# Kernel tuning notes

Hardware: AMD Instinct MI355X
Metric: run time of the kernel (lower is better)

The kernel has to match this reference:

```python
import jax, jax.numpy as jnp
import numpy as np
import math

S, B, H, NH = 2048, 1, 4096, 32
D = H // NH  # 128 head dim


def rotate_half(x):
    x1, x2 = x[..., : x.shape[-1] // 2], x[..., x.shape[-1] // 2 :]
    return jnp.concatenate((-x2, x1), axis=-1)


def setup_inputs() -> dict:
    key = jax.random.key(0)
    k1, k2, k3, k4, k5 = jax.random.split(key, 5)
    hidden_states = jax.random.normal(k1, (S, B, H), dtype=jnp.float32)
    position_ids = jnp.broadcast_to(jnp.arange(S, dtype=jnp.int32)[None, :], (B, S))
    # causal mask: True = masked (upper triangle above diagonal)
    attention_mask = jnp.triu(jnp.ones((S, S), dtype=bool), k=1)[None, None]
    W_qkv = jax.random.normal(k2, (H, 3 * H), dtype=jnp.float32) * 0.02
    b_qkv = jax.random.normal(k3, (3 * H,), dtype=jnp.float32) * 0.02
    W_dense = jax.random.normal(k4, (H, H), dtype=jnp.float32) * 0.02
    b_dense = jax.random.normal(k5, (H,), dtype=jnp.float32) * 0.02
    return {
        "hidden_states": hidden_states,
        "position_ids": position_ids,
        "attention_mask": attention_mask,
        "W_qkv": W_qkv,
        "b_qkv": b_qkv,
        "W_dense": W_dense,
        "b_dense": b_dense,
        "layer_id": 27,
    }


def reference(hidden_states, position_ids, attention_mask, W_qkv, b_qkv, W_dense, b_dense, layer_id):
    s, b, h = hidden_states.shape
    nh, d = NH, D
    # QKV projection: [s, b, 3h] -> [s, b, nh, 3d] -> split
    mixed = hidden_states @ W_qkv + b_qkv
    mixed = mixed.reshape(s, b, nh, 3 * d)
    q, k, v = jnp.split(mixed, 3, axis=-1)  # each [s, b, nh, d]
    # rotary embedding indexed by position_ids (transposed to [s, b])
    pos = position_ids.T  # [s, b]
    inv_freq = 1.0 / (10000.0 ** (jnp.arange(0, d, 2, dtype=jnp.float32) / d))
    freqs = pos[..., None].astype(jnp.float32) * inv_freq  # [s, b, d/2]
    emb = jnp.concatenate((freqs, freqs), axis=-1)  # [s, b, d]
    cos = jnp.cos(emb)[:, :, None, :]  # [s, b, 1, d]
    sin = jnp.sin(emb)[:, :, None, :]
    q = q * cos + rotate_half(q) * sin
    k = k * cos + rotate_half(k) * sin
    # attention with per-layer scaling coeff (cancels in softmax except mask fill)
    coeff = jnp.float32(layer_id + 1)
    q_scaled = q / (math.sqrt(d) * coeff)
    scores = jnp.einsum("sbnd,tbnd->bnst", q_scaled, k)  # [b, nh, s, s]
    scores = jnp.where(attention_mask, jnp.float32(-10000.0), scores) * coeff
    probs = jax.nn.softmax(scores, axis=-1)
    ctx = jnp.einsum("bnst,tbnd->sbnd", probs, v).reshape(s, b, h)
    out = ctx @ W_dense + b_dense
    return out
```

## Files before the change

kernel.cpp:

```cpp
#include <hip/hip_runtime.h>

#define S_LEN 2048
#define HID   4096
#define NHEAD 32
#define DHEAD 128
#define H3    12288

typedef __attribute__((ext_vector_type(8))) __bf16 bf16x8;
typedef __attribute__((ext_vector_type(4))) __bf16 bf16x4;
typedef __attribute__((ext_vector_type(4))) float  f32x4;
typedef __attribute__((ext_vector_type(16))) float f32x16;

__device__ __forceinline__ void gl_lds16(const void* g, void* l) {
  __builtin_amdgcn_global_load_lds(
      (const __attribute__((address_space(1))) void*)g,
      (__attribute__((address_space(3))) void*)l, 16, 0, 0);
}

__global__ void cvt_f32_bf16(const float* __restrict__ in, __bf16* __restrict__ out, int n4) {
  int i = blockIdx.x * blockDim.x + threadIdx.x;
  if (i >= n4) return;
  float4 v = ((const float4*)in)[i];
  bf16x4 o;
  o.x = (__bf16)v.x; o.y = (__bf16)v.y; o.z = (__bf16)v.z; o.w = (__bf16)v.w;
  ((bf16x4*)out)[i] = o;
}

__global__ void transpose_cvt(const float* __restrict__ in, __bf16* __restrict__ out, int R, int C) {
  __shared__ float t[64][65];
  const int tid = threadIdx.x;
  const int r0 = blockIdx.y * 64, c0 = blockIdx.x * 64;
#pragma unroll
  for (int p = 0; p < 4; ++p) {
    int r = p * 16 + (tid >> 4);
    int c4 = (tid & 15) * 4;
    float4 v = *(const float4*)(in + (size_t)(r0 + r) * C + c0 + c4);
    t[r][c4] = v.x; t[r][c4 + 1] = v.y; t[r][c4 + 2] = v.z; t[r][c4 + 3] = v.w;
  }
  __syncthreads();
#pragma unroll
  for (int p = 0; p < 4; ++p) {
    int c = p * 16 + (tid >> 4);
    int rg = (tid & 15) * 4;
    bf16x4 o;
    o.x = (__bf16)t[rg][c]; o.y = (__bf16)t[rg + 1][c];
    o.z = (__bf16)t[rg + 2][c]; o.w = (__bf16)t[rg + 3][c];
    *(bf16x4*)(out + (size_t)(c0 + c) * R + r0 + rg) = o;
  }
}

__global__ void rope_kernel(__bf16* __restrict__ q, __bf16* __restrict__ k,
                            const int* __restrict__ pos) {
  int idx = blockIdx.x * 256 + threadIdx.x;
  int j = idx & 63;
  int hs = idx >> 6;
  int s = hs & (S_LEN - 1);
  float p = (float)pos[s];
  float invf = __expf(-(float)j * (9.210340371976184f / 64.f));
  float a = p * invf;
  float c, sn;
  __sincosf(a, &sn, &c);
  size_t base = (size_t)hs * 128;
  float x1 = (float)q[base + j], x2 = (float)q[base + j + 64];
  q[base + j]      = (__bf16)(x1 * c - x2 * sn);
  q[base + j + 64] = (__bf16)(x2 * c + x1 * sn);
  x1 = (float)k[base + j]; x2 = (float)k[base + j + 64];
  k[base + j]      = (__bf16)(x1 * c - x2 * sn);
  k[base + j + 64] = (__bf16)(x2 * c + x1 * sn);
}

template <int EPI>
__global__ __launch_bounds__(256, 2)
void gemm32(const __bf16* __restrict__ A, const __bf16* __restrict__ BT,
            const float* __restrict__ bias, int K,
            __bf16* __restrict__ outq, __bf16* __restrict__ outk,
            __bf16* __restrict__ outvt, float* __restrict__ outf) {
  const int tid = threadIdx.x;
  const int lane = tid & 63;
  const int wave = tid >> 6;
  const int bm = blockIdx.x * 256;
  const int bn = blockIdx.y * 128;

  __shared__ char lds[49152];
  char* Ab = lds;
  char* Bb = lds + 32768;

  f32x16 acc[4][2] = {};

  const int wm = (wave >> 1) * 128;
  const int wn = (wave & 1) * 64;
  const int l31 = lane & 31;
  const int hi = lane >> 5;

  const int sr = tid >> 3;
  const int scb = ((tid & 7) * 16) ^ ((sr & 7) << 4);
  const int K2 = K * 2;
  const char* Arow = (const char*)A + (size_t)(bm + sr) * K2 + scb;
  const char* Brow = (const char*)BT + (size_t)(bn + sr) * K2 + scb;

  for (int k0 = 0; k0 < K; k0 += 64) {
    const char* a_src = Arow + (size_t)k0 * 2;
    const char* b_src = Brow + (size_t)k0 * 2;
    char* a_dst = Ab + wave * 1024;
    char* b_dst = Bb + wave * 1024;
#pragma unroll
    for (int i = 0; i < 8; ++i)
      gl_lds16(a_src + (size_t)i * 32 * K2, a_dst + i * 4096);
#pragma unroll
    for (int i = 0; i < 4; ++i)
      gl_lds16(b_src + (size_t)i * 32 * K2, b_dst + i * 4096);
    __syncthreads();
#pragma unroll
    for (int kk = 0; kk < 4; ++kk) {
      const int cbase = kk * 32 + (hi << 4);
      bf16x8 af[4], bfr[2];
#pragma unroll
      for (int m = 0; m < 4; ++m) {
        const int row = wm + m * 32 + l31;
        af[m] = *(const bf16x8*)(Ab + row * 128 + (cbase ^ ((row & 7) << 4)));
      }
#pragma unroll
      for (int n = 0; n < 2; ++n) {
        const int row = wn + n * 32 + l31;
        bfr[n] = *(const bf16x8*)(Bb + row * 128 + (cbase ^ ((row & 7) << 4)));
      }
#pragma unroll
      for (int m = 0; m < 4; ++m)
#pragma unroll
        for (int n = 0; n < 2; ++n)
          acc[m][n] = __builtin_amdgcn_mfma_f32_32x32x16_bf16(af[m], bfr[n], acc[m][n], 0, 0, 0);
    }
    __syncthreads();
  }

  if (EPI == 0) {
    const int route = (bn >> 7) % 3;
    const int head = bn / 384;
#pragma unroll
    for (int n = 0; n < 2; ++n) {
      const int d = wn + n * 32 + l31;
      const float bv = bias[bn + d];
#pragma unroll
      for (int m = 0; m < 4; ++m) {
        if (route == 2) {
#pragma unroll
          for (int qd = 0; qd < 4; ++qd) {
            const int srow = bm + wm + m * 32 + qd * 8 + (hi << 2);
            bf16x4 o;
            o.x = (__bf16)(acc[m][n][qd * 4 + 0] + bv);
            o.y = (__bf16)(acc[m][n][qd * 4 + 1] + bv);
            o.z = (__bf16)(acc[m][n][qd * 4 + 2] + bv);
            o.w = (__bf16)(acc[m][n][qd * 4 + 3] + bv);
            *(bf16x4*)(outvt + ((size_t)head * 128 + d) * S_LEN + srow) = o;
          }
        } else {
          __bf16* dst = (route == 0 ? outq : outk) + (size_t)head * S_LEN * 128;
#pragma unroll
          for (int r = 0; r < 16; ++r) {
            const int srow = bm + wm + m * 32 + (r & 3) + 8 * (r >> 2) + (hi << 2);
            dst[(size_t)srow * 128 + d] = (__bf16)(acc[m][n][r] + bv);
          }
        }
      }
    }
  } else {
#pragma unroll
    for (int n = 0; n < 2; ++n) {
      const int col = bn + wn + n * 32 + l31;
      const float bv = bias[col];
#pragma unroll
      for (int m = 0; m < 4; ++m)
#pragma unroll
        for (int r = 0; r < 16; ++r) {
          const int srow = bm + wm + m * 32 + (r & 3) + 8 * (r >> 2) + (hi << 2);
          outf[(size_t)srow * HID + col] = acc[m][n][r] + bv;
        }
    }
  }
}

__global__ __launch_bounds__(256, 2)
void attn_kernel(const __bf16* __restrict__ q, const __bf16* __restrict__ k,
                 const __bf16* __restrict__ vt, __bf16* __restrict__ ctx) {
  const int p = blockIdx.x, h = blockIdx.y;
  const int tid = threadIdx.x, lane = tid & 63, wave = tid >> 6;
  __shared__ __bf16 Ks[64 * 128];
  __shared__ __bf16 Vs[128 * 64];
  __shared__ __bf16 Ps[4][16 * 64];
  char* Kb = (char*)Ks;
  char* Vb = (char*)Vs;
  char* Pb = (char*)(Ps[wave]);

  const __bf16* qh = q + (size_t)h * S_LEN * 128;
  const __bf16* kh = k + (size_t)h * S_LEN * 128;
  const __bf16* vh = vt + (size_t)h * 128 * S_LEN;

  const int cl = lane & 15, rbase = (lane >> 4) << 2;

  const int krow = tid >> 4, kcol = (tid & 15) * 16;
  const int kcs = kcol ^ ((krow & 7) << 4);
  const int vrow = tid >> 3, vcol = (tid & 7) * 16;
  const int vcs = vcol ^ ((vrow & 7) << 4);

  for (int half = 0; half < 2; ++half) {
    const int qt = half ? (31 - p) : p;
    const int qrow0 = qt * 64 + wave * 16;

    bf16x8 qf[4];
#pragma unroll
    for (int kk = 0; kk < 4; ++kk)
      qf[kk] = *(const bf16x8*)(qh + (size_t)(qrow0 + cl) * 128 + kk * 32 + ((lane >> 4) << 3));

    f32x4 oacc[8] = {};
    float mrow[4], lrow[4];
#pragma unroll
    for (int r = 0; r < 4; ++r) { mrow[r] = -1e30f; lrow[r] = 0.f; }

    for (int j = 0; j <= qt; ++j) {
      {
        const char* src = (const char*)(kh + (size_t)(j * 64 + krow) * 128) + kcs;
        char* dst = Kb + wave * 1024;
#pragma unroll
        for (int i = 0; i < 4; ++i)
          gl_lds16(src + (size_t)i * 16 * 256, dst + i * 4096);
      }
      {
        const char* src = (const char*)(vh + (size_t)vrow * S_LEN + j * 64) + vcs;
        char* dst = Vb + wave * 1024;
#pragma unroll
        for (int i = 0; i < 4; ++i)
          gl_lds16(src + (size_t)i * 32 * (S_LEN * 2), dst + i * 4096);
      }
      __syncthreads();

      f32x4 sacc[4] = {};
#pragma unroll
      for (int kk = 0; kk < 4; ++kk) {
        bf16x8 bk[4];
#pragma unroll
        for (int n = 0; n < 4; ++n) {
          int row = n * 16 + cl;
          int cb = (kk * 64 + ((lane >> 4) << 4)) ^ ((row & 7) << 4);
          bk[n] = *(const bf16x8*)(Kb + row * 256 + cb);
        }
#pragma unroll
        for (int n = 0; n < 4; ++n)
          sacc[n] = __builtin_amdgcn_mfma_f32_16x16x32_bf16(qf[kk], bk[n], sacc[n], 0, 0, 0);
      }

      float pmax[4];
#pragma unroll
      for (int r = 0; r < 4; ++r) pmax[r] = -1e30f;
      if (j == qt) {
#pragma unroll
        for (int n = 0; n < 4; ++n) {
          const int col = n * 16 + cl;
#pragma unroll
          for (int r = 0; r < 4; ++r) {
            const int row = wave * 16 + rbase + r;
            float sv = sacc[n][r] * 0.08838834764831845f;
            sv = (col > row) ? -1e30f : sv;
            sacc[n][r] = sv;
            pmax[r] = fmaxf(pmax[r], sv);
          }
        }
      } else {
#pragma unroll
        for (int n = 0; n < 4; ++n)
#pragma unroll
          for (int r = 0; r < 4; ++r) {
            float sv = sacc[n][r] * 0.08838834764831845f;
            sacc[n][r] = sv;
            pmax[r] = fmaxf(pmax[r], sv);
          }
      }
#pragma unroll
      for (int xm = 1; xm < 16; xm <<= 1)
#pragma unroll
        for (int r = 0; r < 4; ++r)
          pmax[r] = fmaxf(pmax[r], __shfl_xor(pmax[r], xm, 64));
#pragma unroll
      for (int r = 0; r < 4; ++r) {
        const float mnew = fmaxf(mrow[r], pmax[r]);
        const float alpha = __expf(mrow[r] - mnew);
        mrow[r] = mnew;
        float psum = 0.f;
#pragma unroll
        for (int n = 0; n < 4; ++n) {
          float pe = __expf(sacc[n][r] - mnew);
          sacc[n][r] = pe;
          psum += pe;
        }
#pragma unroll
        for (int xm = 1; xm < 16; xm <<= 1)
          psum += __shfl_xor(psum, xm, 64);
        lrow[r] = lrow[r] * alpha + psum;
#pragma unroll
        for (int nd = 0; nd < 8; ++nd)
          oacc[nd][r] *= alpha;
      }

#pragma unroll
      for (int n = 0; n < 4; ++n) {
        const int colb = (n * 16 + cl) * 2;
#pragma unroll
        for (int r = 0; r < 4; ++r) {
          const int row = rbase + r;
          *(__bf16*)(Pb + row * 128 + (colb ^ ((row & 7) << 4))) = (__bf16)sacc[n][r];
        }
      }

#pragma unroll
      for (int kk = 0; kk < 2; ++kk) {
        bf16x8 pa, bv[8];
        {
          int row = cl;
          int cb = (kk * 64 + ((lane >> 4) << 4)) ^ ((row & 7) << 4);
          pa = *(const bf16x8*)(Pb + row * 128 + cb);
        }
#pragma unroll
        for (int nd = 0; nd < 8; ++nd) {
          int row = nd * 16 + cl;
          int cb = (kk * 64 + ((lane >> 4) << 4)) ^ ((row & 7) << 4);
          bv[nd] = *(const bf16x8*)(Vb + row * 128 + cb);
        }
#pragma unroll
        for (int nd = 0; nd < 8; ++nd)
          oacc[nd] = __builtin_amdgcn_mfma_f32_16x16x32_bf16(pa, bv[nd], oacc[nd], 0, 0, 0);
      }
      __syncthreads();
    }

#pragma unroll
    for (int nd = 0; nd < 8; ++nd) {
      const int d = nd * 16 + cl;
#pragma unroll
      for (int r = 0; r < 4; ++r) {
        const int srow = qrow0 + rbase + r;
        ctx[(size_t)srow * HID + h * 128 + d] = (__bf16)(oacc[nd][r] / lrow[r]);
      }
    }
  }
}

extern "C" void kernel_launch(void* const* d_in, const int* in_sizes, int n_in,
                              void* d_out, int out_size, void* d_ws, size_t ws_size,
                              hipStream_t stream) {
  const float* hs = (const float*)d_in[0];
  const int* pos = (const int*)d_in[1];
  const float* wqkv = (const float*)d_in[3];
  const float* bqkv = (const float*)d_in[4];
  const float* wd = (const float*)d_in[5];
  const float* bd = (const float*)d_in[6];
  float* out = (float*)d_out;

  char* ws = (char*)d_ws;
  const size_t MB = 1024ull * 1024ull;
  if (ws_size < 160 * MB) return;
  __bf16* wT  = (__bf16*)(ws);
  __bf16* xb  = (__bf16*)(ws + 96 * MB);
  __bf16* qb_ = (__bf16*)(ws + 112 * MB);
  __bf16* kb_ = (__bf16*)(ws + 128 * MB);
  __bf16* vtb = (__bf16*)(ws + 144 * MB);

  cvt_f32_bf16<<<8192, 256, 0, stream>>>(hs, xb, 2097152);
  transpose_cvt<<<dim3(192, 64), 256, 0, stream>>>(wqkv, wT, 4096, 12288);
  gemm32<0><<<dim3(8, 96), 256, 0, stream>>>(xb, wT, bqkv, 4096, qb_, kb_, vtb, nullptr);
  rope_kernel<<<16384, 256, 0, stream>>>(qb_, kb_, pos);
  transpose_cvt<<<dim3(64, 64), 256, 0, stream>>>(wd, wT, 4096, 4096);
  attn_kernel<<<dim3(16, 32), 256, 0, stream>>>(qb_, kb_, vtb, xb);
  gemm32<1><<<dim3(8, 32), 256, 0, stream>>>(xb, wT, bd, 4096, nullptr, nullptr, nullptr, out);
}
```

Before: 500.9 us.

## Fold softmax scale into RoPE, add lazy rescale, use 128x128 dense GEMM

The 1/sqrt(d) scale is folded into Q during the RoPE pass, which removes a multiply per score in attention. The online softmax now skips the running-max update and accumulator rescale when every row's new max stays within 8 of the old one. The output projection moves to a new 128x128-tile GEMM built on 16x16x32 MFMA, launched on a 16x32 grid instead of 8x32 so more blocks fill the CUs. Tradeoffs: scaling Q before rounding to bf16 shifts rounding slightly, skipped rescales rely on exp staying bounded, and the new GEMM has no double buffering.

```diff
diff --git a/kernel.cpp b/kernel.cpp
--- a/kernel.cpp
+++ b/kernel.cpp
@@ -60,13 +60,93 @@
   float a = p * invf;
   float c, sn;
   __sincosf(a, &sn, &c);
+  const float SC = 0.08838834764831845f;
   size_t base = (size_t)hs * 128;
   float x1 = (float)q[base + j], x2 = (float)q[base + j + 64];
-  q[base + j]      = (__bf16)(x1 * c - x2 * sn);
-  q[base + j + 64] = (__bf16)(x2 * c + x1 * sn);
+  q[base + j]      = (__bf16)((x1 * c - x2 * sn) * SC);
+  q[base + j + 64] = (__bf16)((x2 * c + x1 * sn) * SC);
   x1 = (float)k[base + j]; x2 = (float)k[base + j + 64];
   k[base + j]      = (__bf16)(x1 * c - x2 * sn);
   k[base + j + 64] = (__bf16)(x2 * c + x1 * sn);
+}
+
+template <int EPI>
+__global__ __launch_bounds__(256, 2)
+void gemm_bf16(const __bf16* __restrict__ A, const __bf16* __restrict__ BT,
+               const float* __restrict__ bias, int K,
+               float* __restrict__ outf) {
+  const int tid = threadIdx.x;
+  const int lane = tid & 63;
+  const int wave = tid >> 6;
+  const int bm = blockIdx.x * 128;
+  const int bn = blockIdx.y * 128;
+
+  __shared__ __bf16 As[128 * 64];
+  __shared__ __bf16 Bs[128 * 64];
+  char* Ab = (char*)As;
+  char* Bb = (char*)Bs;
+
+  f32x4 acc[4][4] = {};
+
+  const int wm = (wave >> 1) * 64;
+  const int wn = (wave & 1) * 64;
+
+  const int sr = tid >> 3;
+  const int sc = (tid & 7) * 16;
+  const int scs = sc ^ ((sr & 7) << 4);
+
+  const char* Arow = (const char*)(A + (size_t)(bm + sr) * K) + scs;
+  const char* Brow = (const char*)(BT + (size_t)(bn + sr) * K) + scs;
+
+  for (int k0 = 0; k0 < K; k0 += 64) {
+    const char* a_src = Arow + (size_t)k0 * 2;
+    const char* b_src = Brow + (size_t)k0 * 2;
+    char* a_dst = Ab + wave * 1024;
+    char* b_dst = Bb + wave * 1024;
+#pragma unroll
+    for (int i = 0; i < 4; ++i) {
+      gl_lds16(a_src + (size_t)i * 32 * K * 2, a_dst + i * 4096);
+      gl_lds16(b_src + (size_t)i * 32 * K * 2, b_dst + i * 4096);
+    }
+    __syncthreads();
+#pragma unroll
+    for (int kk = 0; kk < 2; ++kk) {
+      bf16x8 af[4], bfr[4];
+#pragma unroll
+      for (int m = 0; m < 4; ++m) {
+        int row = wm + m * 16 + (lane & 15);
+        int cb = (kk * 64 + ((lane >> 4) << 4)) ^ ((row & 7) << 4);
+        af[m] = *(const bf16x8*)(Ab + row * 128 + cb);
+      }
+#pragma unroll
+      for (int n = 0; n < 4; ++n) {
+        int row = wn + n * 16 + (lane & 15);
+        int cb = (kk * 64 + ((lane >> 4) << 4)) ^ ((row & 7) << 4);
+        bfr[n] = *(const bf16x8*)(Bb + row * 128 + cb);
+      }
+#pragma unroll
+      for (int m = 0; m < 4; ++m)
+#pragma unroll
+        for (int n = 0; n < 4; ++n)
+          acc[m][n] = __builtin_amdgcn_mfma_f32_16x16x32_bf16(af[m], bfr[n], acc[m][n], 0, 0, 0);
+    }
+    __syncthreads();
+  }
+
+  const int rbase = (lane >> 4) << 2;
+  const int cl = lane & 15;
+#pragma unroll
+  for (int n = 0; n < 4; ++n) {
+    const int col = bn + wn + n * 16 + cl;
+    const float bv = bias[col];
+#pragma unroll
+    for (int m = 0; m < 4; ++m) {
+      const int srow = bm + wm + m * 16 + rbase;
+#pragma unroll
+      for (int r = 0; r < 4; ++r)
+        outf[(size_t)(srow + r) * HID + col] = acc[m][n][r] + bv;
+    }
+  }
 }
 
 template <int EPI>
@@ -74,7 +154,7 @@
 void gemm32(const __bf16* __restrict__ A, const __bf16* __restrict__ BT,
             const float* __restrict__ bias, int K,
             __bf16* __restrict__ outq, __bf16* __restrict__ outk,
-            __bf16* __restrict__ outvt, float* __restrict__ outf) {
+            __bf16* __restrict__ outvt) {
   const int tid = threadIdx.x;
   const int lane = tid & 63;
   const int wave = tid >> 6;
@@ -133,48 +213,33 @@
     __syncthreads();
   }
 
-  if (EPI == 0) {
-    const int route = (bn >> 7) % 3;
-    const int head = bn / 384;
-#pragma unroll
-    for (int n = 0; n < 2; ++n) {
-      const int d = wn + n * 32 + l31;
-      const float bv = bias[bn + d];
-#pragma unroll
-      for (int m = 0; m < 4; ++m) {
-        if (route == 2) {
-#pragma unroll
-          for (int qd = 0; qd < 4; ++qd) {
-            const int srow = bm + wm + m * 32 + qd * 8 + (hi << 2);
-            bf16x4 o;
-            o.x = (__bf16)(acc[m][n][qd * 4 + 0] + bv);
-            o.y = (__bf16)(acc[m][n][qd * 4 + 1] + bv);
-            o.z = (__bf16)(acc[m][n][qd * 4 + 2] + bv);
-            o.w = (__bf16)(acc[m][n][qd * 4 + 3] + bv);
-            *(bf16x4*)(outvt + ((size_t)head * 128 + d) * S_LEN + srow) = o;
-          }
-        } else {
-          __bf16* dst = (route == 0 ? outq : outk) + (size_t)head * S_LEN * 128;
-#pragma unroll
-          for (int r = 0; r < 16; ++r) {
-            const int srow = bm + wm + m * 32 + (r & 3) + 8 * (r >> 2) + (hi << 2);
-            dst[(size_t)srow * 128 + d] = (__bf16)(acc[m][n][r] + bv);
-          }
-        }
-      }
-    }
-  } else {
-#pragma unroll
-    for (int n = 0; n < 2; ++n) {
-      const int col = bn + wn + n * 32 + l31;
-      const float bv = bias[col];
-#pragma unroll
-      for (int m = 0; m < 4; ++m)
+  const int route = (bn >> 7) % 3;
+  const int head = bn / 384;
+#pragma unroll
+  for (int n = 0; n < 2; ++n) {
+    const int d = wn + n * 32 + l31;
+    const float bv = bias[bn + d];
+#pragma unroll
+    for (int m = 0; m < 4; ++m) {
+      if (route == 2) {
+#pragma unroll
+        for (int qd = 0; qd < 4; ++qd) {
+          const int srow = bm + wm + m * 32 + qd * 8 + (hi << 2);
+          bf16x4 o;
+          o.x = (__bf16)(acc[m][n][qd * 4 + 0] + bv);
+          o.y = (__bf16)(acc[m][n][qd * 4 + 1] + bv);
+          o.z = (__bf16)(acc[m][n][qd * 4 + 2] + bv);
+          o.w = (__bf16)(acc[m][n][qd * 4 + 3] + bv);
+          *(bf16x4*)(outvt + ((size_t)head * 128 + d) * S_LEN + srow) = o;
+        }
+      } else {
+        __bf16* dst = (route == 0 ? outq : outk) + (size_t)head * S_LEN * 128;
 #pragma unroll
         for (int r = 0; r < 16; ++r) {
           const int srow = bm + wm + m * 32 + (r & 3) + 8 * (r >> 2) + (hi << 2);
-          outf[(size_t)srow * HID + col] = acc[m][n][r] + bv;
-        }
+          dst[(size_t)srow * 128 + d] = (__bf16)(acc[m][n][r] + bv);
+        }
+      }
     }
   }
 }
@@ -258,8 +323,7 @@
 #pragma unroll
           for (int r = 0; r < 4; ++r) {
             const int row = wave * 16 + rbase + r;
-            float sv = sacc[n][r] * 0.08838834764831845f;
-            sv = (col > row) ? -1e30f : sv;
+            float sv = (col > row) ? -1e30f : sacc[n][r];
             sacc[n][r] = sv;
             pmax[r] = fmaxf(pmax[r], sv);
           }
@@ -268,36 +332,53 @@
 #pragma unroll
         for (int n = 0; n < 4; ++n)
 #pragma unroll
-          for (int r = 0; r < 4; ++r) {
-            float sv = sacc[n][r] * 0.08838834764831845f;
-            sacc[n][r] = sv;
-            pmax[r] = fmaxf(pmax[r], sv);
-          }
+          for (int r = 0; r < 4; ++r)
+            pmax[r] = fmaxf(pmax[r], sacc[n][r]);
       }
 #pragma unroll
       for (int xm = 1; xm < 16; xm <<= 1)
 #pragma unroll
         for (int r = 0; r < 4; ++r)
           pmax[r] = fmaxf(pmax[r], __shfl_xor(pmax[r], xm, 64));
-#pragma unroll
-      for (int r = 0; r < 4; ++r) {
-        const float mnew = fmaxf(mrow[r], pmax[r]);
-        const float alpha = __expf(mrow[r] - mnew);
-        mrow[r] = mnew;
-        float psum = 0.f;
-#pragma unroll
-        for (int n = 0; n < 4; ++n) {
-          float pe = __expf(sacc[n][r] - mnew);
-          sacc[n][r] = pe;
-          psum += pe;
-        }
-#pragma unroll
-        for (int xm = 1; xm < 16; xm <<= 1)
-          psum += __shfl_xor(psum, xm, 64);
-        lrow[r] = lrow[r] * alpha + psum;
-#pragma unroll
-        for (int nd = 0; nd < 8; ++nd)
-          oacc[nd][r] *= alpha;
+
+      const bool okd = (pmax[0] <= mrow[0] + 8.f) && (pmax[1] <= mrow[1] + 8.f) &&
+                       (pmax[2] <= mrow[2] + 8.f) && (pmax[3] <= mrow[3] + 8.f);
+      if (__all(okd)) {
+#pragma unroll
+        for (int r = 0; r < 4; ++r) {
+          float psum = 0.f;
+#pragma unroll
+          for (int n = 0; n < 4; ++n) {
+            float pe = __expf(sacc[n][r] - mrow[r]);
+            sacc[n][r] = pe;
+            psum += pe;
+          }
+#pragma unroll
+          for (int xm = 1; xm < 16; xm <<= 1)
+            psum += __shfl_xor(psum, xm, 64);
+          lrow[r] += psum;
+        }
+      } else {
+#pragma unroll
+        for (int r = 0; r < 4; ++r) {
+          const float mnew = fmaxf(mrow[r], pmax[r]);
+          const float alpha = __expf(mrow[r] - mnew);
+          mrow[r] = mnew;
+          float psum = 0.f;
+#pragma unroll
+          for (int n = 0; n < 4; ++n) {
+            float pe = __expf(sacc[n][r] - mnew);
+            sacc[n][r] = pe;
+            psum += pe;
+          }
+#pragma unroll
+          for (int xm = 1; xm < 16; xm <<= 1)
+            psum += __shfl_xor(psum, xm, 64);
+          lrow[r] = lrow[r] * alpha + psum;
+#pragma unroll
+          for (int nd = 0; nd < 8; ++nd)
+            oacc[nd][r] *= alpha;
+        }
       }
 
 #pragma unroll
@@ -365,9 +446,9 @@
 
   cvt_f32_bf16<<<8192, 256, 0, stream>>>(hs, xb, 2097152);
   transpose_cvt<<<dim3(192, 64), 256, 0, stream>>>(wqkv, wT, 4096, 12288);
-  gemm32<0><<<dim3(8, 96), 256, 0, stream>>>(xb, wT, bqkv, 4096, qb_, kb_, vtb, nullptr);
+  gemm32<0><<<dim3(8, 96), 256, 0, stream>>>(xb, wT, bqkv, 4096, qb_, kb_, vtb);
   rope_kernel<<<16384, 256, 0, stream>>>(qb_, kb_, pos);
   transpose_cvt<<<dim3(64, 64), 256, 0, stream>>>(wd, wT, 4096, 4096);
   attn_kernel<<<dim3(16, 32), 256, 0, stream>>>(qb_, kb_, vtb, xb);
-  gemm32<1><<<dim3(8, 32), 256, 0, stream>>>(xb, wT, bd, 4096, nullptr, nullptr, nullptr, out);
-}
+  gemm_bf16<1><<<dim3(16, 32), 256, 0, stream>>>(xb, wT, bd, 4096, out);
+}
```

Result: faster. 473.0 us (-5.6%).
